# Performance work log

Measured on AMD Instinct MI355X. Metric: run time of the kernel, lower is better.

Reference implementation:

```python
import jax, jax.numpy as jnp
import numpy as np

DIM = 768
NUM_HEAD = 12
DIM_HEAD = DIM // NUM_HEAD
SCALE = DIM_HEAD ** -0.5
B, N = 4, 1024


def setup_inputs() -> dict:
    key = jax.random.key(0)
    ks = jax.random.split(key, 6)
    return {
        "x": jax.random.normal(ks[0], (B, N, DIM), jnp.float32),
        "q_weight": jax.random.normal(ks[1], (DIM, DIM), jnp.float32) * 0.02,
        "k_weight": jax.random.normal(ks[2], (DIM, DIM), jnp.float32) * 0.02,
        "v_weight": jax.random.normal(ks[3], (DIM, DIM), jnp.float32) * 0.02,
        "q_bias": jnp.zeros((DIM,), jnp.float32),
        "k_bias": jnp.zeros((DIM,), jnp.float32),
        "v_bias": jnp.zeros((DIM,), jnp.float32),
        "proj_weight": jax.random.normal(ks[4], (DIM, DIM), jnp.float32) * 0.02,
        "proj_bias": jax.random.normal(ks[5], (DIM,), jnp.float32) * 0.02,
    }


def reference(x, q_weight, k_weight, v_weight, q_bias, k_bias, v_bias,
              proj_weight, proj_bias):
    B_, N_, C = x.shape
    shortcut = x
    # pre-norm: torch .std() is unbiased (ddof=1)
    mean = jnp.mean(x, axis=-1, keepdims=True)
    std = jnp.std(x, axis=-1, keepdims=True, ddof=1)
    xn = (x - mean) / std
    # F.linear: x @ W.T + b
    q = xn @ q_weight.T + q_bias
    k = xn @ k_weight.T + k_bias
    v = xn @ v_weight.T + v_bias
    # b n (h d) -> b h n d
    q = q.reshape(B_, N_, NUM_HEAD, DIM_HEAD).transpose(0, 2, 1, 3)
    k = k.reshape(B_, N_, NUM_HEAD, DIM_HEAD).transpose(0, 2, 1, 3)
    v = v.reshape(B_, N_, NUM_HEAD, DIM_HEAD).transpose(0, 2, 1, 3)
    attn = jnp.einsum('bhqd,bhkd->bhqk', q, k * SCALE)
    attn = jax.nn.softmax(attn, axis=-1)
    out = jnp.einsum('bhqk,bhkd->bhqd', attn, v)
    out = out.transpose(0, 2, 1, 3).reshape(B_, N_, C)
    out = out @ proj_weight.T + proj_bias
    return out + shortcut
```

## Files before the change

kernel.cpp:

```cpp
#include <hip/hip_runtime.h>

typedef unsigned short ushort_t;
typedef unsigned int uint_t;
typedef __attribute__((ext_vector_type(8))) unsigned short ushort8;
typedef __attribute__((ext_vector_type(2))) unsigned int uint2v;
typedef __attribute__((ext_vector_type(8))) __bf16 bf16x8;
typedef __attribute__((ext_vector_type(4))) float floatx4;

#define DIM 768
#define NHEAD 12
#define DHEAD 64
#define SEQ 1024
#define BATCH 4
#define TOKENS (BATCH * SEQ)
#define WELEM (DIM * DIM)
#define SCALE_LOG2E 0.18033688011112042f

static __device__ __forceinline__ uint_t fbits(float f) {
  union { float f; uint_t u; } c; c.f = f; return c.u;
}
static __device__ __forceinline__ ushort_t f2bf(float f) {
  return (ushort_t)((fbits(f) + 0x8000u) >> 16);
}
static __device__ __forceinline__ uint_t pack_bf2(float lo, float hi) {
  const uint_t a = fbits(lo) + 0x8000u, b = fbits(hi) + 0x8000u;
#if __has_builtin(__builtin_amdgcn_perm)
  return __builtin_amdgcn_perm(b, a, 0x07060302u);
#else
  return (a >> 16) | (b & 0xFFFF0000u);
#endif
}
static __device__ __forceinline__ floatx4 mfma16(ushort8 a, ushort8 b, floatx4 c) {
  return __builtin_amdgcn_mfma_f32_16x16x32_bf16(
      __builtin_bit_cast(bf16x8, a), __builtin_bit_cast(bf16x8, b), c, 0, 0, 0);
}
static __device__ __forceinline__ void gload_lds16(const ushort_t* g,
                                                   ushort_t* l) {
  __builtin_amdgcn_global_load_lds(
      (const __attribute__((address_space(1))) void*)g,
      (__attribute__((address_space(3))) void*)l, 16, 0, 0);
}

__global__ __launch_bounds__(256) void cvt_kernel(
    const float* __restrict__ qw, const float* __restrict__ kw,
    const float* __restrict__ vw, const float* __restrict__ pw,
    ushort_t* __restrict__ dst) {
  const float* s = (blockIdx.y == 0) ? qw : (blockIdx.y == 1) ? kw
                  : (blockIdx.y == 2) ? vw : pw;
  ushort_t* d = dst + (size_t)blockIdx.y * WELEM;
  const int i = (blockIdx.x * 256 + threadIdx.x) * 4;
  const float4 f = *(const float4*)&s[i];
  uint2v o;
  o[0] = pack_bf2(f.x, f.y);
  o[1] = pack_bf2(f.z, f.w);
  *(uint2v*)&d[i] = o;
}

__global__ __launch_bounds__(256) void ln_kernel(const float* __restrict__ x,
                                                 ushort_t* __restrict__ xn) {
  const int wave = threadIdx.x >> 6, lane = threadIdx.x & 63;
  const int row = blockIdx.x * 4 + wave;
  const float4* xr = (const float4*)(x + (size_t)row * DIM);
  float4 v[3];
  float s = 0.f, s2 = 0.f;
#pragma unroll
  for (int j = 0; j < 3; ++j) {
    v[j] = xr[j * 64 + lane];
    s += v[j].x + v[j].y + v[j].z + v[j].w;
    s2 += v[j].x * v[j].x + v[j].y * v[j].y + v[j].z * v[j].z + v[j].w * v[j].w;
  }
#pragma unroll
  for (int off = 1; off < 64; off <<= 1) {
    s += __shfl_xor(s, off);
    s2 += __shfl_xor(s2, off);
  }
  const float mean = s * (1.f / 768.f);
  const float var = (s2 - 768.f * mean * mean) * (1.f / 767.f);
  const float rstd = rsqrtf(var);
  ushort_t* xo = xn + (size_t)row * DIM;
#pragma unroll
  for (int j = 0; j < 3; ++j) {
    uint2v o;
    o[0] = pack_bf2((v[j].x - mean) * rstd, (v[j].y - mean) * rstd);
    o[1] = pack_bf2((v[j].z - mean) * rstd, (v[j].w - mean) * rstd);
    *(uint2v*)&xo[(j * 64 + lane) * 4] = o;
  }
}

#define BK 64
__global__ __launch_bounds__(256) void qkv_kernel(
    const ushort_t* __restrict__ xn, const ushort_t* __restrict__ wbf,
    const float* __restrict__ qb, const float* __restrict__ kb,
    const float* __restrict__ vb,
    ushort_t* __restrict__ qh, ushort_t* __restrict__ kh,
    ushort_t* __restrict__ vh) {
  __shared__ ushort_t As[128 * BK];
  __shared__ ushort_t Bs[128 * BK];
  const int tid = threadIdx.x;
  const int wave = tid >> 6, lane = tid & 63, quad = lane >> 4, l15 = lane & 15;
  const int m0 = blockIdx.x * 128;
  const int mat = blockIdx.y / 6, nb = blockIdx.y % 6;
  const int n0 = nb * 128;
  const ushort_t* W = wbf + (size_t)mat * WELEM;
  const float* bias = (mat == 0) ? qb : (mat == 1) ? kb : vb;
  ushort_t* dst = (mat == 0) ? qh : (mat == 1) ? kh : vh;
  const float oscale = (mat == 0) ? SCALE_LOG2E : 1.0f;
  const int wm = (wave >> 1) * 64, wn = (wave & 1) * 64;
  const int srow = lane >> 3;
  const int schunk = (lane & 7) ^ srow;
  const int l7 = l15 & 7;

  floatx4 acc[4][4];
#pragma unroll
  for (int i = 0; i < 4; ++i)
#pragma unroll
    for (int j = 0; j < 4; ++j) acc[i][j] = (floatx4){0.f, 0.f, 0.f, 0.f};

  for (int k0 = 0; k0 < DIM; k0 += BK) {
#pragma unroll
    for (int i = 0; i < 4; ++i) {
      const int c = wave * 4 + i;
      const int row = c * 8 + srow;
      gload_lds16(&xn[(size_t)(m0 + row) * DIM + k0 + schunk * 8], &As[c * 512]);
      gload_lds16(&W[(size_t)(n0 + row) * DIM + k0 + schunk * 8], &Bs[c * 512]);
    }
    __syncthreads();
    ushort8 af[4][2], bfr[4][2];
#pragma unroll
    for (int i = 0; i < 4; ++i)
#pragma unroll
      for (int kh = 0; kh < 2; ++kh) {
        const int ch = ((kh * 4 + quad) ^ l7) * 8;
        af[i][kh] = *(const ushort8*)&As[(wm + i * 16 + l15) * BK + ch];
        bfr[i][kh] = *(const ushort8*)&Bs[(wn + i * 16 + l15) * BK + ch];
      }
#pragma unroll
    for (int kh = 0; kh < 2; ++kh)
#pragma unroll
      for (int i = 0; i < 4; ++i)
#pragma unroll
        for (int j = 0; j < 4; ++j)
          acc[i][j] = mfma16(af[i][kh], bfr[j][kh], acc[i][j]);
    __syncthreads();
  }

#pragma unroll
  for (int i = 0; i < 4; ++i) {
#pragma unroll
    for (int j = 0; j < 4; ++j) {
      const int col = n0 + wn + j * 16 + l15;
      const float bv = bias[col];
      const int hh = col >> 6, d = col & 63;
#pragma unroll
      for (int r = 0; r < 4; ++r) {
        const int rowg = m0 + wm + i * 16 + quad * 4 + r;
        const int bb = rowg >> 10, nn = rowg & 1023;
        dst[(size_t)(((bb * NHEAD + hh) * SEQ) + nn) * DHEAD + d] =
            f2bf((acc[i][j][r] + bv) * oscale);
      }
    }
  }
}

#define KSTR 66
#define PSTR 68
__global__ __launch_bounds__(256) void attn_kernel(
    const ushort_t* __restrict__ qh, const ushort_t* __restrict__ kh,
    const ushort_t* __restrict__ vh, ushort_t* __restrict__ ao) {
  __shared__ ushort_t Ks[64 * 64];
  __shared__ ushort_t Vts[64 * KSTR];
  __shared__ ushort_t Ps[4][16 * PSTR];
  const int tid = threadIdx.x;
  const int wave = tid >> 6, lane = tid & 63, quad = lane >> 4, l15 = lane & 15;
  const int h = blockIdx.y, b = blockIdx.z;
  const int basekv = ((b * NHEAD + h) * SEQ) * DHEAD;
  const int q0 = blockIdx.x * 64 + wave * 16;
  const int l7 = l15 & 7;

  ushort8 qf[2];
  {
    const ushort_t* Qr = qh + basekv + (q0 + l15) * DHEAD;
    qf[0] = *(const ushort8*)&Qr[quad * 8];
    qf[1] = *(const ushort8*)&Qr[32 + quad * 8];
  }
  ushort8 ones;
#pragma unroll
  for (int i = 0; i < 8; ++i) ones[i] = 0x3F80;

  floatx4 o[4];
#pragma unroll
  for (int t = 0; t < 4; ++t) o[t] = (floatx4){0.f, 0.f, 0.f, 0.f};
  floatx4 acc_l = (floatx4){0.f, 0.f, 0.f, 0.f};

  const int ksrow = lane >> 3, kschunk = (lane & 7) ^ ksrow;
  const int vp = tid >> 3, vcc = tid & 7;
  const int vl = vp & 15, vs0 = (vp >> 4) << 1;
  const int kA = vs0 * 16 + vl;

  for (int kt = 0; kt < SEQ; kt += 64) {
#pragma unroll
    for (int i = 0; i < 2; ++i) {
      const int c = wave * 2 + i;
      gload_lds16(&kh[basekv + (kt + c * 8 + ksrow) * DHEAD + kschunk * 8],
                  &Ks[c * 512]);
    }
    {
      const ushort8 vA =
          *(const ushort8*)&vh[basekv + (kt + kA) * DHEAD + vcc * 8];
      const ushort8 vB =
          *(const ushort8*)&vh[basekv + (kt + kA + 16) * DHEAD + vcc * 8];
#pragma unroll
      for (int j = 0; j < 8; ++j)
        *(uint_t*)&Vts[(vcc * 8 + j) * KSTR + vl * 4 + vs0] =
            (uint_t)vA[j] | ((uint_t)vB[j] << 16);
    }
    __syncthreads();

    floatx4 sacc[4];
#pragma unroll
    for (int s = 0; s < 4; ++s) sacc[s] = (floatx4){0.f, 0.f, 0.f, 0.f};
#pragma unroll
    for (int s = 0; s < 4; ++s) {
#pragma unroll
      for (int hh = 0; hh < 2; ++hh) {
        const ushort8 kf = *(const ushort8*)&Ks[(s * 16 + l15) * 64 +
                                                (((hh * 4 + quad) ^ l7) * 8)];
        sacc[s] = mfma16(qf[hh], kf, sacc[s]);
      }
    }

#pragma unroll
    for (int r = 0; r < 4; ++r) {
      uint2v pk;
      pk[0] = pack_bf2(exp2f(sacc[0][r]), exp2f(sacc[1][r]));
      pk[1] = pack_bf2(exp2f(sacc[2][r]), exp2f(sacc[3][r]));
      *(uint2v*)&Ps[wave][(quad * 4 + r) * PSTR + l15 * 4] = pk;
    }

#pragma unroll
    for (int hh = 0; hh < 2; ++hh) {
      const ushort8 pf =
          *(const ushort8*)&Ps[wave][l15 * PSTR + hh * 32 + quad * 8];
      acc_l = mfma16(pf, ones, acc_l);
#pragma unroll
      for (int t = 0; t < 4; ++t) {
        const ushort8 vf =
            *(const ushort8*)&Vts[(t * 16 + l15) * KSTR + hh * 32 + quad * 8];
        o[t] = mfma16(pf, vf, o[t]);
      }
    }
    __syncthreads();
  }

#pragma unroll
  for (int r = 0; r < 4; ++r) {
    const float rl = 1.f / acc_l[r];
    const int qrow = q0 + quad * 4 + r;
    const int token = b * SEQ + qrow;
#pragma unroll
    for (int t = 0; t < 4; ++t)
      ao[(size_t)token * DIM + h * DHEAD + t * 16 + l15] = f2bf(o[t][r] * rl);
  }
}

__global__ __launch_bounds__(256) void proj_kernel(
    const ushort_t* __restrict__ ao, const ushort_t* __restrict__ pwb,
    const float* __restrict__ pb, const float* __restrict__ x,
    float* __restrict__ out) {
  __shared__ ushort_t As[128 * BK];
  __shared__ ushort_t Bs[128 * BK];
  const int tid = threadIdx.x;
  const int wave = tid >> 6, lane = tid & 63, quad = lane >> 4, l15 = lane & 15;
  const int m0 = blockIdx.x * 128;
  const int n0 = blockIdx.y * 128;
  const int wm = (wave >> 1) * 64, wn = (wave & 1) * 64;
  const int srow = lane >> 3;
  const int schunk = (lane & 7) ^ srow;
  const int l7 = l15 & 7;

  floatx4 acc[4][4];
#pragma unroll
  for (int i = 0; i < 4; ++i)
#pragma unroll
    for (int j = 0; j < 4; ++j) acc[i][j] = (floatx4){0.f, 0.f, 0.f, 0.f};

  for (int k0 = 0; k0 < DIM; k0 += BK) {
#pragma unroll
    for (int i = 0; i < 4; ++i) {
      const int c = wave * 4 + i;
      const int row = c * 8 + srow;
      gload_lds16(&ao[(size_t)(m0 + row) * DIM + k0 + schunk * 8], &As[c * 512]);
      gload_lds16(&pwb[(size_t)(n0 + row) * DIM + k0 + schunk * 8], &Bs[c * 512]);
    }
    __syncthreads();
    ushort8 af[4][2], bfr[4][2];
#pragma unroll
    for (int i = 0; i < 4; ++i)
#pragma unroll
      for (int kh = 0; kh < 2; ++kh) {
        const int ch = ((kh * 4 + quad) ^ l7) * 8;
        af[i][kh] = *(const ushort8*)&As[(wm + i * 16 + l15) * BK + ch];
        bfr[i][kh] = *(const ushort8*)&Bs[(wn + i * 16 + l15) * BK + ch];
      }
#pragma unroll
    for (int kh = 0; kh < 2; ++kh)
#pragma unroll
      for (int i = 0; i < 4; ++i)
#pragma unroll
        for (int j = 0; j < 4; ++j)
          acc[i][j] = mfma16(af[i][kh], bfr[j][kh], acc[i][j]);
    __syncthreads();
  }

#pragma unroll
  for (int i = 0; i < 4; ++i) {
#pragma unroll
    for (int j = 0; j < 4; ++j) {
      const int col = n0 + wn + j * 16 + l15;
      const float bv = pb[col];
#pragma unroll
      for (int r = 0; r < 4; ++r) {
        const int rowg = m0 + wm + i * 16 + quad * 4 + r;
        out[(size_t)rowg * DIM + col] =
            acc[i][j][r] + bv + x[(size_t)rowg * DIM + col];
      }
    }
  }
}

extern "C" void kernel_launch(void* const* d_in, const int* in_sizes, int n_in,
                              void* d_out, int out_size, void* d_ws,
                              size_t ws_size, hipStream_t stream) {
  const float* x  = (const float*)d_in[0];
  const float* qw = (const float*)d_in[1];
  const float* kw = (const float*)d_in[2];
  const float* vw = (const float*)d_in[3];
  const float* qb = (const float*)d_in[4];
  const float* kb = (const float*)d_in[5];
  const float* vb = (const float*)d_in[6];
  const float* pw = (const float*)d_in[7];
  const float* pb = (const float*)d_in[8];
  float* out = (float*)d_out;

  ushort_t* ws = (ushort_t*)d_ws;
  const size_t NTOK = (size_t)TOKENS * DIM;
  ushort_t* xn  = ws;
  ushort_t* qh  = ws + NTOK;
  ushort_t* kh  = ws + 2 * NTOK;
  ushort_t* vh  = ws + 3 * NTOK;
  ushort_t* wbf = ws + 4 * NTOK;
  ushort_t* ao  = xn;

  cvt_kernel<<<dim3(WELEM / 1024, 4), 256, 0, stream>>>(qw, kw, vw, pw, wbf);
  ln_kernel<<<TOKENS / 4, 256, 0, stream>>>(x, xn);
  qkv_kernel<<<dim3(32, 18), 256, 0, stream>>>(xn, wbf, qb, kb, vb, qh, kh, vh);
  attn_kernel<<<dim3(16, NHEAD, BATCH), 256, 0, stream>>>(qh, kh, vh, ao);
  proj_kernel<<<dim3(32, 6), 256, 0, stream>>>(ao, wbf + 3 * (size_t)WELEM, pb,
                                               x, out);
}
```

Measured before the change: 170.6 us.

## Emit V pre-transposed from QKV GEMM, widen attention waves, shrink proj tiles

The QKV kernel now computes V with swapped MFMA operands and writes it in a transposed, pre-permuted layout, so the attention kernel can load V tiles with direct global-to-LDS copies instead of a manual register transpose. The attention kernel drops to 128 threads, with each wave handling two 16-row query tiles so every loaded K/V fragment feeds twice as many MFMAs. The projection GEMM uses 64-row M tiles to double its block count for better CU occupancy. The trade-offs are more registers per wave in attention, more scattered V stores in the QKV epilogue, and more blocks each loading the same weights in the projection.

```diff
diff --git a/kernel.cpp b/kernel.cpp
--- a/kernel.cpp
+++ b/kernel.cpp
@@ -93,7 +93,7 @@
     const float* __restrict__ qb, const float* __restrict__ kb,
     const float* __restrict__ vb,
     ushort_t* __restrict__ qh, ushort_t* __restrict__ kh,
-    ushort_t* __restrict__ vh) {
+    ushort_t* __restrict__ vt) {
   __shared__ ushort_t As[128 * BK];
   __shared__ ushort_t Bs[128 * BK];
   const int tid = threadIdx.x;
@@ -102,12 +102,9 @@
   const int mat = blockIdx.y / 6, nb = blockIdx.y % 6;
   const int n0 = nb * 128;
   const ushort_t* W = wbf + (size_t)mat * WELEM;
-  const float* bias = (mat == 0) ? qb : (mat == 1) ? kb : vb;
-  ushort_t* dst = (mat == 0) ? qh : (mat == 1) ? kh : vh;
-  const float oscale = (mat == 0) ? SCALE_LOG2E : 1.0f;
   const int wm = (wave >> 1) * 64, wn = (wave & 1) * 64;
-  const int srow = lane >> 3;
-  const int schunk = (lane & 7) ^ srow;
+  const int srow8 = lane >> 3;
+  const int schunk = (lane & 7) ^ srow8;
   const int l7 = l15 & 7;
 
   floatx4 acc[4][4];
@@ -120,7 +117,7 @@
 #pragma unroll
     for (int i = 0; i < 4; ++i) {
       const int c = wave * 4 + i;
-      const int row = c * 8 + srow;
+      const int row = c * 8 + srow8;
       gload_lds16(&xn[(size_t)(m0 + row) * DIM + k0 + schunk * 8], &As[c * 512]);
       gload_lds16(&W[(size_t)(n0 + row) * DIM + k0 + schunk * 8], &Bs[c * 512]);
     }
@@ -129,137 +126,178 @@
 #pragma unroll
     for (int i = 0; i < 4; ++i)
 #pragma unroll
-      for (int kh = 0; kh < 2; ++kh) {
-        const int ch = ((kh * 4 + quad) ^ l7) * 8;
-        af[i][kh] = *(const ushort8*)&As[(wm + i * 16 + l15) * BK + ch];
-        bfr[i][kh] = *(const ushort8*)&Bs[(wn + i * 16 + l15) * BK + ch];
-      }
-#pragma unroll
-    for (int kh = 0; kh < 2; ++kh)
-#pragma unroll
-      for (int i = 0; i < 4; ++i)
-#pragma unroll
-        for (int j = 0; j < 4; ++j)
-          acc[i][j] = mfma16(af[i][kh], bfr[j][kh], acc[i][j]);
-    __syncthreads();
-  }
-
-#pragma unroll
-  for (int i = 0; i < 4; ++i) {
-#pragma unroll
-    for (int j = 0; j < 4; ++j) {
-      const int col = n0 + wn + j * 16 + l15;
-      const float bv = bias[col];
-      const int hh = col >> 6, d = col & 63;
-#pragma unroll
-      for (int r = 0; r < 4; ++r) {
-        const int rowg = m0 + wm + i * 16 + quad * 4 + r;
-        const int bb = rowg >> 10, nn = rowg & 1023;
-        dst[(size_t)(((bb * NHEAD + hh) * SEQ) + nn) * DHEAD + d] =
-            f2bf((acc[i][j][r] + bv) * oscale);
-      }
-    }
-  }
-}
-
-#define KSTR 66
+      for (int k2 = 0; k2 < 2; ++k2) {
+        const int ch = ((k2 * 4 + quad) ^ l7) * 8;
+        af[i][k2] = *(const ushort8*)&As[(wm + i * 16 + l15) * BK + ch];
+        bfr[i][k2] = *(const ushort8*)&Bs[(wn + i * 16 + l15) * BK + ch];
+      }
+    if (mat != 2) {
+#pragma unroll
+      for (int k2 = 0; k2 < 2; ++k2)
+#pragma unroll
+        for (int i = 0; i < 4; ++i)
+#pragma unroll
+          for (int j = 0; j < 4; ++j)
+            acc[i][j] = mfma16(af[i][k2], bfr[j][k2], acc[i][j]);
+    } else {
+#pragma unroll
+      for (int k2 = 0; k2 < 2; ++k2)
+#pragma unroll
+        for (int i = 0; i < 4; ++i)
+#pragma unroll
+          for (int j = 0; j < 4; ++j)
+            acc[i][j] = mfma16(bfr[i][k2], af[j][k2], acc[i][j]);
+    }
+    __syncthreads();
+  }
+
+  if (mat != 2) {
+    const float* bias = (mat == 0) ? qb : kb;
+    ushort_t* dst = (mat == 0) ? qh : kh;
+    const float oscale = (mat == 0) ? SCALE_LOG2E : 1.0f;
+#pragma unroll
+    for (int i = 0; i < 4; ++i) {
+#pragma unroll
+      for (int j = 0; j < 4; ++j) {
+        const int col = n0 + wn + j * 16 + l15;
+        const float bv = bias[col];
+        const int hh = col >> 6, d = col & 63;
+#pragma unroll
+        for (int r = 0; r < 4; ++r) {
+          const int rowg = m0 + wm + i * 16 + quad * 4 + r;
+          const int bb = rowg >> 10, nn = rowg & 1023;
+          dst[(size_t)(((bb * NHEAD + hh) * SEQ) + nn) * DHEAD + d] =
+              f2bf((acc[i][j][r] + bv) * oscale);
+        }
+      }
+    }
+  } else {
+#pragma unroll
+    for (int i = 0; i < 4; ++i) {
+#pragma unroll
+      for (int j = 0; j < 4; ++j) {
+        const int tokb = m0 + wm + j * 16;
+        const int tok = tokb + l15;
+        const int bb = tok >> 10, nn = tok & 1023;
+        const int t2 = (nn >> 4) & 3;
+        const int goff = (nn & ~63) + l15 * 4 + t2;
+#pragma unroll
+        for (int r = 0; r < 4; ++r) {
+          const int ch = n0 + wn + i * 16 + quad * 4 + r;
+          const int hh = ch >> 6, d = ch & 63;
+          vt[(size_t)(((bb * NHEAD + hh) * DHEAD) + d) * SEQ + goff] =
+              f2bf(acc[i][j][r] + vb[ch]);
+        }
+      }
+    }
+  }
+}
+
 #define PSTR 68
-__global__ __launch_bounds__(256) void attn_kernel(
+__global__ __launch_bounds__(128) void attn_kernel(
     const ushort_t* __restrict__ qh, const ushort_t* __restrict__ kh,
-    const ushort_t* __restrict__ vh, ushort_t* __restrict__ ao) {
+    const ushort_t* __restrict__ vt, ushort_t* __restrict__ ao) {
   __shared__ ushort_t Ks[64 * 64];
-  __shared__ ushort_t Vts[64 * KSTR];
-  __shared__ ushort_t Ps[4][16 * PSTR];
+  __shared__ ushort_t Vts[64 * 64];
+  __shared__ ushort_t Ps[2][2][16 * PSTR];
   const int tid = threadIdx.x;
   const int wave = tid >> 6, lane = tid & 63, quad = lane >> 4, l15 = lane & 15;
+  const int l7 = l15 & 7;
   const int h = blockIdx.y, b = blockIdx.z;
   const int basekv = ((b * NHEAD + h) * SEQ) * DHEAD;
-  const int q0 = blockIdx.x * 64 + wave * 16;
-  const int l7 = l15 & 7;
-
-  ushort8 qf[2];
-  {
-    const ushort_t* Qr = qh + basekv + (q0 + l15) * DHEAD;
-    qf[0] = *(const ushort8*)&Qr[quad * 8];
-    qf[1] = *(const ushort8*)&Qr[32 + quad * 8];
+  const int basevt = ((b * NHEAD + h) * DHEAD) * SEQ;
+  const int q0 = blockIdx.x * 64 + wave * 32;
+
+  ushort8 qf[2][2];
+#pragma unroll
+  for (int w = 0; w < 2; ++w) {
+    const ushort_t* Qr = qh + basekv + (q0 + w * 16 + l15) * DHEAD;
+    qf[w][0] = *(const ushort8*)&Qr[quad * 8];
+    qf[w][1] = *(const ushort8*)&Qr[32 + quad * 8];
   }
   ushort8 ones;
 #pragma unroll
   for (int i = 0; i < 8; ++i) ones[i] = 0x3F80;
 
-  floatx4 o[4];
-#pragma unroll
-  for (int t = 0; t < 4; ++t) o[t] = (floatx4){0.f, 0.f, 0.f, 0.f};
-  floatx4 acc_l = (floatx4){0.f, 0.f, 0.f, 0.f};
-
-  const int ksrow = lane >> 3, kschunk = (lane & 7) ^ ksrow;
-  const int vp = tid >> 3, vcc = tid & 7;
-  const int vl = vp & 15, vs0 = (vp >> 4) << 1;
-  const int kA = vs0 * 16 + vl;
+  floatx4 o[2][4];
+#pragma unroll
+  for (int w = 0; w < 2; ++w)
+#pragma unroll
+    for (int t = 0; t < 4; ++t) o[w][t] = (floatx4){0.f, 0.f, 0.f, 0.f};
+  floatx4 acc_l[2] = {(floatx4){0.f, 0.f, 0.f, 0.f},
+                      (floatx4){0.f, 0.f, 0.f, 0.f}};
+
+  const int srow8 = lane >> 3, schunk = (lane & 7) ^ srow8;
 
   for (int kt = 0; kt < SEQ; kt += 64) {
 #pragma unroll
-    for (int i = 0; i < 2; ++i) {
-      const int c = wave * 2 + i;
-      gload_lds16(&kh[basekv + (kt + c * 8 + ksrow) * DHEAD + kschunk * 8],
+    for (int i = 0; i < 4; ++i) {
+      const int c = wave * 4 + i;
+      gload_lds16(&kh[basekv + (kt + c * 8 + srow8) * DHEAD + schunk * 8],
                   &Ks[c * 512]);
-    }
-    {
-      const ushort8 vA =
-          *(const ushort8*)&vh[basekv + (kt + kA) * DHEAD + vcc * 8];
-      const ushort8 vB =
-          *(const ushort8*)&vh[basekv + (kt + kA + 16) * DHEAD + vcc * 8];
-#pragma unroll
-      for (int j = 0; j < 8; ++j)
-        *(uint_t*)&Vts[(vcc * 8 + j) * KSTR + vl * 4 + vs0] =
-            (uint_t)vA[j] | ((uint_t)vB[j] << 16);
-    }
-    __syncthreads();
-
-    floatx4 sacc[4];
-#pragma unroll
-    for (int s = 0; s < 4; ++s) sacc[s] = (floatx4){0.f, 0.f, 0.f, 0.f};
+      gload_lds16(&vt[basevt + (c * 8 + srow8) * SEQ + kt + schunk * 8],
+                  &Vts[c * 512]);
+    }
+    __syncthreads();
+
+    floatx4 sacc[2][4];
+#pragma unroll
+    for (int w = 0; w < 2; ++w)
+#pragma unroll
+      for (int s = 0; s < 4; ++s) sacc[w][s] = (floatx4){0.f, 0.f, 0.f, 0.f};
 #pragma unroll
     for (int s = 0; s < 4; ++s) {
 #pragma unroll
       for (int hh = 0; hh < 2; ++hh) {
         const ushort8 kf = *(const ushort8*)&Ks[(s * 16 + l15) * 64 +
                                                 (((hh * 4 + quad) ^ l7) * 8)];
-        sacc[s] = mfma16(qf[hh], kf, sacc[s]);
-      }
-    }
-
+#pragma unroll
+        for (int w = 0; w < 2; ++w)
+          sacc[w][s] = mfma16(qf[w][hh], kf, sacc[w][s]);
+      }
+    }
+
+#pragma unroll
+    for (int w = 0; w < 2; ++w) {
+#pragma unroll
+      for (int r = 0; r < 4; ++r) {
+        uint2v pk;
+        pk[0] = pack_bf2(exp2f(sacc[w][0][r]), exp2f(sacc[w][1][r]));
+        pk[1] = pack_bf2(exp2f(sacc[w][2][r]), exp2f(sacc[w][3][r]));
+        *(uint2v*)&Ps[wave][w][(quad * 4 + r) * PSTR + l15 * 4] = pk;
+      }
+    }
+
+#pragma unroll
+    for (int hh = 0; hh < 2; ++hh) {
+      ushort8 pf[2];
+#pragma unroll
+      for (int w = 0; w < 2; ++w) {
+        pf[w] = *(const ushort8*)&Ps[wave][w][l15 * PSTR + hh * 32 + quad * 8];
+        acc_l[w] = mfma16(pf[w], ones, acc_l[w]);
+      }
+#pragma unroll
+      for (int t = 0; t < 4; ++t) {
+        const ushort8 vf = *(const ushort8*)&Vts[(t * 16 + l15) * 64 +
+                                                 (((hh * 4 + quad) ^ l7) * 8)];
+#pragma unroll
+        for (int w = 0; w < 2; ++w) o[w][t] = mfma16(pf[w], vf, o[w][t]);
+      }
+    }
+    __syncthreads();
+  }
+
+#pragma unroll
+  for (int w = 0; w < 2; ++w) {
 #pragma unroll
     for (int r = 0; r < 4; ++r) {
-      uint2v pk;
-      pk[0] = pack_bf2(exp2f(sacc[0][r]), exp2f(sacc[1][r]));
-      pk[1] = pack_bf2(exp2f(sacc[2][r]), exp2f(sacc[3][r]));
-      *(uint2v*)&Ps[wave][(quad * 4 + r) * PSTR + l15 * 4] = pk;
-    }
-
-#pragma unroll
-    for (int hh = 0; hh < 2; ++hh) {
-      const ushort8 pf =
-          *(const ushort8*)&Ps[wave][l15 * PSTR + hh * 32 + quad * 8];
-      acc_l = mfma16(pf, ones, acc_l);
-#pragma unroll
-      for (int t = 0; t < 4; ++t) {
-        const ushort8 vf =
-            *(const ushort8*)&Vts[(t * 16 + l15) * KSTR + hh * 32 + quad * 8];
-        o[t] = mfma16(pf, vf, o[t]);
-      }
-    }
-    __syncthreads();
-  }
-
-#pragma unroll
-  for (int r = 0; r < 4; ++r) {
-    const float rl = 1.f / acc_l[r];
-    const int qrow = q0 + quad * 4 + r;
-    const int token = b * SEQ + qrow;
-#pragma unroll
-    for (int t = 0; t < 4; ++t)
-      ao[(size_t)token * DIM + h * DHEAD + t * 16 + l15] = f2bf(o[t][r] * rl);
+      const float rl = 1.f / acc_l[w][r];
+      const int token = b * SEQ + q0 + w * 16 + quad * 4 + r;
+#pragma unroll
+      for (int t = 0; t < 4; ++t)
+        ao[(size_t)token * DIM + h * DHEAD + t * 16 + l15] =
+            f2bf(o[w][t][r] * rl);
+    }
   }
 }
 
@@ -267,53 +305,60 @@
     const ushort_t* __restrict__ ao, const ushort_t* __restrict__ pwb,
     const float* __restrict__ pb, const float* __restrict__ x,
     float* __restrict__ out) {
-  __shared__ ushort_t As[128 * BK];
+  __shared__ ushort_t As[64 * BK];
   __shared__ ushort_t Bs[128 * BK];
   const int tid = threadIdx.x;
   const int wave = tid >> 6, lane = tid & 63, quad = lane >> 4, l15 = lane & 15;
-  const int m0 = blockIdx.x * 128;
+  const int m0 = blockIdx.x * 64;
   const int n0 = blockIdx.y * 128;
-  const int wm = (wave >> 1) * 64, wn = (wave & 1) * 64;
-  const int srow = lane >> 3;
-  const int schunk = (lane & 7) ^ srow;
+  const int wm = (wave >> 1) * 32, wn = (wave & 1) * 64;
+  const int srow8 = lane >> 3;
+  const int schunk = (lane & 7) ^ srow8;
   const int l7 = l15 & 7;
 
-  floatx4 acc[4][4];
-#pragma unroll
-  for (int i = 0; i < 4; ++i)
+  floatx4 acc[2][4];
+#pragma unroll
+  for (int i = 0; i < 2; ++i)
 #pragma unroll
     for (int j = 0; j < 4; ++j) acc[i][j] = (floatx4){0.f, 0.f, 0.f, 0.f};
 
   for (int k0 = 0; k0 < DIM; k0 += BK) {
+#pragma unroll
+    for (int i = 0; i < 2; ++i) {
+      const int c = wave * 2 + i;
+      const int row = c * 8 + srow8;
+      gload_lds16(&ao[(size_t)(m0 + row) * DIM + k0 + schunk * 8], &As[c * 512]);
+    }
 #pragma unroll
     for (int i = 0; i < 4; ++i) {
       const int c = wave * 4 + i;
-      const int row = c * 8 + srow;
-      gload_lds16(&ao[(size_t)(m0 + row) * DIM + k0 + schunk * 8], &As[c * 512]);
+      const int row = c * 8 + srow8;
       gload_lds16(&pwb[(size_t)(n0 + row) * DIM + k0 + schunk * 8], &Bs[c * 512]);
     }
     __syncthreads();
-    ushort8 af[4][2], bfr[4][2];
-#pragma unroll
-    for (int i = 0; i < 4; ++i)
-#pragma unroll
-      for (int kh = 0; kh < 2; ++kh) {
-        const int ch = ((kh * 4 + quad) ^ l7) * 8;
-        af[i][kh] = *(const ushort8*)&As[(wm + i * 16 + l15) * BK + ch];
-        bfr[i][kh] = *(const ushort8*)&Bs[(wn + i * 16 + l15) * BK + ch];
-      }
-#pragma unroll
-    for (int kh = 0; kh < 2; ++kh)
-#pragma unroll
-      for (int i = 0; i < 4; ++i)
+    ushort8 af[2][2], bfr[4][2];
+#pragma unroll
+    for (int k2 = 0; k2 < 2; ++k2) {
+      const int ch = ((k2 * 4 + quad) ^ l7) * 8;
+#pragma unroll
+      for (int i = 0; i < 2; ++i)
+        af[i][k2] = *(const ushort8*)&As[(wm + i * 16 + l15) * BK + ch];
+#pragma unroll
+      for (int j = 0; j < 4; ++j)
+        bfr[j][k2] = *(const ushort8*)&Bs[(wn + j * 16 + l15) * BK + ch];
+    }
+#pragma unroll
+    for (int k2 = 0; k2 < 2; ++k2)
+#pragma unroll
+      for (int i = 0; i < 2; ++i)
 #pragma unroll
         for (int j = 0; j < 4; ++j)
-          acc[i][j] = mfma16(af[i][kh], bfr[j][kh], acc[i][j]);
-    __syncthreads();
-  }
-
-#pragma unroll
-  for (int i = 0; i < 4; ++i) {
+          acc[i][j] = mfma16(af[i][k2], bfr[j][k2], acc[i][j]);
+    __syncthreads();
+  }
+
+#pragma unroll
+  for (int i = 0; i < 2; ++i) {
 #pragma unroll
     for (int j = 0; j < 4; ++j) {
       const int col = n0 + wn + j * 16 + l15;
@@ -347,14 +392,14 @@
   ushort_t* xn  = ws;
   ushort_t* qh  = ws + NTOK;
   ushort_t* kh  = ws + 2 * NTOK;
-  ushort_t* vh  = ws + 3 * NTOK;
+  ushort_t* vt  = ws + 3 * NTOK;
   ushort_t* wbf = ws + 4 * NTOK;
   ushort_t* ao  = xn;
 
   cvt_kernel<<<dim3(WELEM / 1024, 4), 256, 0, stream>>>(qw, kw, vw, pw, wbf);
   ln_kernel<<<TOKENS / 4, 256, 0, stream>>>(x, xn);
-  qkv_kernel<<<dim3(32, 18), 256, 0, stream>>>(xn, wbf, qb, kb, vb, qh, kh, vh);
-  attn_kernel<<<dim3(16, NHEAD, BATCH), 256, 0, stream>>>(qh, kh, vh, ao);
-  proj_kernel<<<dim3(32, 6), 256, 0, stream>>>(ao, wbf + 3 * (size_t)WELEM, pb,
+  qkv_kernel<<<dim3(32, 18), 256, 0, stream>>>(xn, wbf, qb, kb, vb, qh, kh, vt);
+  attn_kernel<<<dim3(16, NHEAD, BATCH), 128, 0, stream>>>(qh, kh, vt, ao);
+  proj_kernel<<<dim3(64, 6), 256, 0, stream>>>(ao, wbf + 3 * (size_t)WELEM, pb,
                                                x, out);
 }
```

Result: no change. 171.0 us (+0.2%).
